# Kernel optimization log

Hardware: AMD Instinct MI355X
Metric: run time of the kernel (lower is better)

## Reference

```python
import jax, jax.numpy as jnp
import numpy as np

E = 8  # num_experts

def setup_inputs() -> dict:
    key = jax.random.key(0)
    ks = jax.random.split(key, 6)
    b, s, d, f = 4, 1024, 1024, 4096
    return {
        "x": jax.random.normal(ks[0], (b, s, d), jnp.float32),
        "Wr": jax.random.normal(ks[1], (d, E), jnp.float32) * 0.02,
        "br": jnp.zeros((E,), jnp.float32),
        "W1": jax.random.normal(ks[2], (E, d, f), jnp.float32) * 0.02,
        "b1": jnp.zeros((E, f), jnp.float32),
        "W2": jax.random.normal(ks[3], (E, f, d), jnp.float32) * 0.02,
        "b2": jnp.zeros((E, d), jnp.float32),
        "k": 2,
    }

def reference(x, Wr, br, W1, b1, W2, b2, k):
    # Router: linear -> softmax -> keep top-k gate probs per token (zero elsewhere).
    # (Gaussian routing noise is a train-time stochastic term; omitted for a
    # deterministic eval-mode reference.)
    logits = jnp.einsum('bsd,de->bse', x, Wr) + br          # [b,s,E]
    probs = jax.nn.softmax(logits, axis=-1)                 # [b,s,E]
    kth = jax.lax.top_k(probs, k)[0][..., -1:]              # [b,s,1]
    gates = jnp.where(probs >= kth, probs, 0.0)             # [b,s,E] sparse gate values
    g = jnp.transpose(gates, (2, 0, 1))[..., None]          # exp_masks [E,b,s,1]

    # Mask-then-dense expert compute, exactly as the torch module:
    # expert_input = x * (mask > 0); out = MLP(expert_input) * gate; sum over experts.
    xm = x[None] * (g > 0).astype(x.dtype)                  # [E,b,s,d]
    h = jax.nn.gelu(jnp.einsum('ebsd,edf->ebsf', xm, W1) + b1[:, None, None, :],
                    approximate=False)                      # [E,b,s,4d]
    out = jnp.einsum('ebsf,efd->ebsd', h, W2) + b2[:, None, None, :]
    out = out * g                                           # gate the expert outputs
    return jnp.sum(out, axis=0)                             # 'sum' aggregation -> [b,s,d]
```

## Files before the change

### kernel.cpp

```cpp
#include <hip/hip_runtime.h>
#include <math.h>

#define T_TOK 4096
#define DDIM  1024
#define FDIM  4096
#define NEXP  8
#define HCAP  8448

typedef __attribute__((ext_vector_type(8))) short bf16x8;
typedef __attribute__((ext_vector_type(4))) float f32x4;

__device__ __forceinline__ unsigned short f2bf(float f) {
  unsigned int u = __float_as_uint(f);
  u += 0x7fffu + ((u >> 16) & 1u);
  return (unsigned short)(u >> 16);
}

__global__ void transpose_cvt_kernel(const float* __restrict__ src,
                                     unsigned short* __restrict__ dst,
                                     int R, int C) {
  __shared__ float tile[32][33];
  int e = blockIdx.z;
  int c0 = blockIdx.x * 32, r0 = blockIdx.y * 32;
  const float* s = src + (size_t)e * R * C;
  unsigned short* d = dst + (size_t)e * R * C;
  int tx = threadIdx.x, ty = threadIdx.y;
#pragma unroll
  for (int i = 0; i < 32; i += 8)
    tile[ty + i][tx] = s[(size_t)(r0 + ty + i) * C + (c0 + tx)];
  __syncthreads();
#pragma unroll
  for (int i = 0; i < 32; i += 8)
    d[(size_t)(c0 + ty + i) * R + (r0 + tx)] = f2bf(tile[tx][ty + i]);
}

__global__ void router_kernel(const float* __restrict__ x, const float* __restrict__ Wr,
                              const float* __restrict__ br, const int* __restrict__ kptr,
                              unsigned short* __restrict__ x_bf,
                              int* __restrict__ counts, int* __restrict__ ids,
                              float* __restrict__ gatev) {
  int t = blockIdx.x * 4 + (threadIdx.x >> 6);
  int lane = threadIdx.x & 63;
  const float* xr = x + (size_t)t * DDIM;
  float acc[NEXP];
#pragma unroll
  for (int e = 0; e < NEXP; ++e) acc[e] = 0.f;
#pragma unroll
  for (int i = 0; i < DDIM / 64; ++i) {
    int idx = lane + 64 * i;
    float xv = xr[idx];
    x_bf[(size_t)t * DDIM + idx] = f2bf(xv);
    const float* wr = Wr + (size_t)idx * NEXP;
#pragma unroll
    for (int e = 0; e < NEXP; ++e) acc[e] += xv * wr[e];
  }
#pragma unroll
  for (int e = 0; e < NEXP; ++e) {
    float v = acc[e];
    for (int off = 32; off > 0; off >>= 1) v += __shfl_xor(v, off);
    acc[e] = v;
  }
  if (lane == 0) {
    float logits[NEXP], probs[NEXP];
    float m = -1e30f;
#pragma unroll
    for (int e = 0; e < NEXP; ++e) { logits[e] = acc[e] + br[e]; m = fmaxf(m, logits[e]); }
    float s = 0.f;
#pragma unroll
    for (int e = 0; e < NEXP; ++e) { probs[e] = expf(logits[e] - m); s += probs[e]; }
    float inv = 1.f / s;
#pragma unroll
    for (int e = 0; e < NEXP; ++e) probs[e] *= inv;
    int kk = *kptr;
    float tmp[NEXP];
#pragma unroll
    for (int e = 0; e < NEXP; ++e) tmp[e] = probs[e];
    float kth = 2.f;
    for (int j = 0; j < kk; ++j) {
      int bi = 0; float bv = -1.f;
#pragma unroll
      for (int e = 0; e < NEXP; ++e)
        if (tmp[e] > bv) { bv = tmp[e]; bi = e; }
      kth = bv; tmp[bi] = -1.f;
    }
#pragma unroll
    for (int e = 0; e < NEXP; ++e) {
      if (probs[e] >= kth) {
        int pos = atomicAdd(&counts[e], 1);
        if (pos < T_TOK) { ids[e * T_TOK + pos] = t; gatev[e * T_TOK + pos] = probs[e]; }
      }
    }
  }
}

__global__ void offsets_kernel(const int* __restrict__ counts, int* __restrict__ hbase) {
  if (threadIdx.x == 0 && blockIdx.x == 0) {
    int s = 0;
    for (int e = 0; e < NEXP; ++e) { hbase[e] = s; s += counts[e]; }
  }
}

__global__ void __launch_bounds__(256) gemm1_kernel(
    const unsigned short* __restrict__ x_bf,
    const unsigned short* __restrict__ W1t,
    const float* __restrict__ b1,
    const int* __restrict__ counts, const int* __restrict__ hbase,
    const int* __restrict__ ids,
    unsigned short* __restrict__ h) {
  int e = blockIdx.z;
  int n_e = counts[e];
  int mt = blockIdx.y;
  if (mt * 128 >= n_e) return;
  int nt = blockIdx.x;
  const unsigned short* Bt = W1t + (size_t)e * FDIM * DDIM;
  __shared__ unsigned short ldsA[128 * 32];
  __shared__ unsigned short ldsB[128 * 32];
  int tid = threadIdx.x;

  const unsigned short* asrc[2];
  const unsigned short* bsrc[2];
  int loff[2];
#pragma unroll
  for (int j = 0; j < 2; ++j) {
    int id = tid + j * 256;
    int row = id >> 2;
    int col = (id & 3) * 8;
    loff[j] = row * 32 + col;
    int gm = mt * 128 + row;
    if (gm > n_e - 1) gm = n_e - 1;
    int tok = ids[e * T_TOK + gm];
    asrc[j] = x_bf + (size_t)tok * DDIM + col;
    bsrc[j] = Bt + (size_t)(nt * 128 + row) * DDIM + col;
  }

  f32x4 acc[4][4];
#pragma unroll
  for (int mi = 0; mi < 4; ++mi)
#pragma unroll
    for (int ni = 0; ni < 4; ++ni) acc[mi][ni] = {0.f, 0.f, 0.f, 0.f};

  int wave = tid >> 6, lane = tid & 63;
  int wm = (wave >> 1) * 64, wn = (wave & 1) * 64;
  int l16 = lane & 15, q = lane >> 4;

  for (int k0 = 0; k0 < DDIM; k0 += 32) {
#pragma unroll
    for (int j = 0; j < 2; ++j) {
      uint4 av = *(const uint4*)(asrc[j] + k0);
      uint4 bv = *(const uint4*)(bsrc[j] + k0);
      *(uint4*)&ldsA[loff[j]] = av;
      *(uint4*)&ldsB[loff[j]] = bv;
    }
    __syncthreads();
    bf16x8 af[4], bfr[4];
#pragma unroll
    for (int mi = 0; mi < 4; ++mi)
      af[mi] = *(const bf16x8*)&ldsA[(wm + mi * 16 + l16) * 32 + q * 8];
#pragma unroll
    for (int ni = 0; ni < 4; ++ni)
      bfr[ni] = *(const bf16x8*)&ldsB[(wn + ni * 16 + l16) * 32 + q * 8];
#pragma unroll
    for (int mi = 0; mi < 4; ++mi)
#pragma unroll
      for (int ni = 0; ni < 4; ++ni)
        acc[mi][ni] = __builtin_amdgcn_mfma_f32_16x16x32_bf16(af[mi], bfr[ni], acc[mi][ni], 0, 0, 0);
    __syncthreads();
  }

  int base = hbase[e];
#pragma unroll
  for (int mi = 0; mi < 4; ++mi) {
#pragma unroll
    for (int r = 0; r < 4; ++r) {
      int rl = wm + mi * 16 + q * 4 + r;
      int gm = mt * 128 + rl;
      if (gm >= n_e) continue;
      int hr = base + gm;
      if (hr >= HCAP) continue;
#pragma unroll
      for (int ni = 0; ni < 4; ++ni) {
        int col = nt * 128 + wn + ni * 16 + l16;
        float v = acc[mi][ni][r] + b1[e * FDIM + col];
        float g = 0.5f * v * (1.0f + erff(v * 0.70710678118654752440f));
        h[(size_t)hr * FDIM + col] = f2bf(g);
      }
    }
  }
}

__global__ void __launch_bounds__(256) gemm2_kernel(
    const unsigned short* __restrict__ h,
    const unsigned short* __restrict__ W2t,
    const float* __restrict__ b2,
    const int* __restrict__ counts, const int* __restrict__ hbase,
    const int* __restrict__ ids, const float* __restrict__ gatev,
    float* __restrict__ out) {
  int e = blockIdx.z;
  int n_e = counts[e];
  int mt = blockIdx.y;
  if (mt * 128 >= n_e) return;
  int nt = blockIdx.x;
  const unsigned short* Bt = W2t + (size_t)e * DDIM * FDIM;
  int base = hbase[e];
  __shared__ unsigned short ldsA[128 * 32];
  __shared__ unsigned short ldsB[128 * 32];
  int tid = threadIdx.x;

  const unsigned short* asrc[2];
  const unsigned short* bsrc[2];
  int loff[2];
#pragma unroll
  for (int j = 0; j < 2; ++j) {
    int id = tid + j * 256;
    int row = id >> 2;
    int col = (id & 3) * 8;
    loff[j] = row * 32 + col;
    int gm = mt * 128 + row;
    if (gm > n_e - 1) gm = n_e - 1;
    int hr = base + gm;
    if (hr > HCAP - 1) hr = HCAP - 1;
    asrc[j] = h + (size_t)hr * FDIM + col;
    bsrc[j] = Bt + (size_t)(nt * 128 + row) * FDIM + col;
  }

  f32x4 acc[4][4];
#pragma unroll
  for (int mi = 0; mi < 4; ++mi)
#pragma unroll
    for (int ni = 0; ni < 4; ++ni) acc[mi][ni] = {0.f, 0.f, 0.f, 0.f};

  int wave = tid >> 6, lane = tid & 63;
  int wm = (wave >> 1) * 64, wn = (wave & 1) * 64;
  int l16 = lane & 15, q = lane >> 4;

  for (int k0 = 0; k0 < FDIM; k0 += 32) {
#pragma unroll
    for (int j = 0; j < 2; ++j) {
      uint4 av = *(const uint4*)(asrc[j] + k0);
      uint4 bv = *(const uint4*)(bsrc[j] + k0);
      *(uint4*)&ldsA[loff[j]] = av;
      *(uint4*)&ldsB[loff[j]] = bv;
    }
    __syncthreads();
    bf16x8 af[4], bfr[4];
#pragma unroll
    for (int mi = 0; mi < 4; ++mi)
      af[mi] = *(const bf16x8*)&ldsA[(wm + mi * 16 + l16) * 32 + q * 8];
#pragma unroll
    for (int ni = 0; ni < 4; ++ni)
      bfr[ni] = *(const bf16x8*)&ldsB[(wn + ni * 16 + l16) * 32 + q * 8];
#pragma unroll
    for (int mi = 0; mi < 4; ++mi)
#pragma unroll
      for (int ni = 0; ni < 4; ++ni)
        acc[mi][ni] = __builtin_amdgcn_mfma_f32_16x16x32_bf16(af[mi], bfr[ni], acc[mi][ni], 0, 0, 0);
    __syncthreads();
  }

#pragma unroll
  for (int mi = 0; mi < 4; ++mi) {
#pragma unroll
    for (int r = 0; r < 4; ++r) {
      int rl = wm + mi * 16 + q * 4 + r;
      int gm = mt * 128 + rl;
      if (gm >= n_e) continue;
      int tok = ids[e * T_TOK + gm];
      float g = gatev[e * T_TOK + gm];
#pragma unroll
      for (int ni = 0; ni < 4; ++ni) {
        int col = nt * 128 + wn + ni * 16 + l16;
        float v = g * (acc[mi][ni][r] + b2[e * DDIM + col]);
        atomicAdd(&out[(size_t)tok * DDIM + col], v);
      }
    }
  }
}

extern "C" void kernel_launch(void* const* d_in, const int* in_sizes, int n_in,
                              void* d_out, int out_size, void* d_ws, size_t ws_size,
                              hipStream_t stream) {
  const float* x  = (const float*)d_in[0];
  const float* Wr = (const float*)d_in[1];
  const float* br = (const float*)d_in[2];
  const float* W1 = (const float*)d_in[3];
  const float* b1 = (const float*)d_in[4];
  const float* W2 = (const float*)d_in[5];
  const float* b2 = (const float*)d_in[6];
  const int* kptr = (const int*)d_in[7];
  float* out = (float*)d_out;

  char* ws = (char*)d_ws;
  size_t o = 0;
  unsigned short* x_bf = (unsigned short*)(ws + o); o += (size_t)T_TOK * DDIM * 2;
  unsigned short* W1t  = (unsigned short*)(ws + o); o += (size_t)NEXP * FDIM * DDIM * 2;
  unsigned short* W2t  = (unsigned short*)(ws + o); o += (size_t)NEXP * DDIM * FDIM * 2;
  unsigned short* hbuf = (unsigned short*)(ws + o); o += (size_t)HCAP * FDIM * 2;
  int*   ids    = (int*)(ws + o);   o += (size_t)NEXP * T_TOK * 4;
  float* gatev  = (float*)(ws + o); o += (size_t)NEXP * T_TOK * 4;
  int*   counts = (int*)(ws + o);   o += 64;
  int*   hbase  = (int*)(ws + o);   o += 64;
  if (o > ws_size) return;

  hipMemsetAsync(d_out, 0, (size_t)out_size * 4, stream);
  hipMemsetAsync(counts, 0, 128, stream);

  transpose_cvt_kernel<<<dim3(FDIM / 32, DDIM / 32, NEXP), dim3(32, 8), 0, stream>>>(W1, W1t, DDIM, FDIM);
  transpose_cvt_kernel<<<dim3(DDIM / 32, FDIM / 32, NEXP), dim3(32, 8), 0, stream>>>(W2, W2t, FDIM, DDIM);

  router_kernel<<<T_TOK / 4, 256, 0, stream>>>(x, Wr, br, kptr, x_bf, counts, ids, gatev);
  offsets_kernel<<<1, 64, 0, stream>>>(counts, hbase);

  gemm1_kernel<<<dim3(FDIM / 128, T_TOK / 128, NEXP), 256, 0, stream>>>(
      x_bf, W1t, b1, counts, hbase, ids, hbuf);
  gemm2_kernel<<<dim3(DDIM / 128, T_TOK / 128, NEXP), 256, 0, stream>>>(
      hbuf, W2t, b2, counts, hbase, ids, gatev, out);
}
```

Before: 752.3 us.

## Use direct global-to-LDS loads and split-K the second expert GEMM

Replaces the register-staged global→LDS tile copies in both expert GEMMs with the global_load_lds builtin, so loads go straight into shared memory without a VGPR round trip. gemm2 is split along the F dimension into two chunks, doubling the grid so more workgroups run at once, with the bias added only by the first chunk and partial results combined through the existing atomicAdd. This adds more atomic traffic to the output and relies on the async LDS load finishing before the existing barrier, with no explicit wait on vmcnt.

```diff
diff --git a/kernel.cpp b/kernel.cpp
--- a/kernel.cpp
+++ b/kernel.cpp
@@ -14,6 +14,13 @@
   unsigned int u = __float_as_uint(f);
   u += 0x7fffu + ((u >> 16) & 1u);
   return (unsigned short)(u >> 16);
+}
+
+__device__ __forceinline__ void async_copy16(const unsigned short* gsrc, unsigned short* ldst) {
+  __builtin_amdgcn_global_load_lds(
+      (const __attribute__((address_space(1))) unsigned int*)gsrc,
+      (__attribute__((address_space(3))) unsigned int*)ldst,
+      16, 0, 0);
 }
 
 __global__ void transpose_cvt_kernel(const float* __restrict__ src,
@@ -146,10 +153,8 @@
   for (int k0 = 0; k0 < DDIM; k0 += 32) {
 #pragma unroll
     for (int j = 0; j < 2; ++j) {
-      uint4 av = *(const uint4*)(asrc[j] + k0);
-      uint4 bv = *(const uint4*)(bsrc[j] + k0);
-      *(uint4*)&ldsA[loff[j]] = av;
-      *(uint4*)&ldsB[loff[j]] = bv;
+      async_copy16(asrc[j] + k0, &ldsA[loff[j]]);
+      async_copy16(bsrc[j] + k0, &ldsB[loff[j]]);
     }
     __syncthreads();
     bf16x8 af[4], bfr[4];
@@ -188,6 +193,8 @@
   }
 }
 
+#define KSPLIT 2
+#define KCHUNK (FDIM / KSPLIT)
 __global__ void __launch_bounds__(256) gemm2_kernel(
     const unsigned short* __restrict__ h,
     const unsigned short* __restrict__ W2t,
@@ -195,12 +202,13 @@
     const int* __restrict__ counts, const int* __restrict__ hbase,
     const int* __restrict__ ids, const float* __restrict__ gatev,
     float* __restrict__ out) {
-  int e = blockIdx.z;
+  int e = blockIdx.z >> 1;
+  int kc = blockIdx.z & 1;
   int n_e = counts[e];
   int mt = blockIdx.y;
   if (mt * 128 >= n_e) return;
   int nt = blockIdx.x;
-  const unsigned short* Bt = W2t + (size_t)e * DDIM * FDIM;
+  const unsigned short* Bt = W2t + (size_t)e * DDIM * FDIM + kc * KCHUNK;
   int base = hbase[e];
   __shared__ unsigned short ldsA[128 * 32];
   __shared__ unsigned short ldsB[128 * 32];
@@ -219,7 +227,7 @@
     if (gm > n_e - 1) gm = n_e - 1;
     int hr = base + gm;
     if (hr > HCAP - 1) hr = HCAP - 1;
-    asrc[j] = h + (size_t)hr * FDIM + col;
+    asrc[j] = h + (size_t)hr * FDIM + kc * KCHUNK + col;
     bsrc[j] = Bt + (size_t)(nt * 128 + row) * FDIM + col;
   }
 
@@ -233,13 +241,11 @@
   int wm = (wave >> 1) * 64, wn = (wave & 1) * 64;
   int l16 = lane & 15, q = lane >> 4;
 
-  for (int k0 = 0; k0 < FDIM; k0 += 32) {
+  for (int k0 = 0; k0 < KCHUNK; k0 += 32) {
 #pragma unroll
     for (int j = 0; j < 2; ++j) {
-      uint4 av = *(const uint4*)(asrc[j] + k0);
-      uint4 bv = *(const uint4*)(bsrc[j] + k0);
-      *(uint4*)&ldsA[loff[j]] = av;
-      *(uint4*)&ldsB[loff[j]] = bv;
+      async_copy16(asrc[j] + k0, &ldsA[loff[j]]);
+      async_copy16(bsrc[j] + k0, &ldsB[loff[j]]);
     }
     __syncthreads();
     bf16x8 af[4], bfr[4];
@@ -269,7 +275,8 @@
 #pragma unroll
       for (int ni = 0; ni < 4; ++ni) {
         int col = nt * 128 + wn + ni * 16 + l16;
-        float v = g * (acc[mi][ni][r] + b2[e * DDIM + col]);
+        float bias = (kc == 0) ? b2[e * DDIM + col] : 0.f;
+        float v = g * (acc[mi][ni][r] + bias);
         atomicAdd(&out[(size_t)tok * DDIM + col], v);
       }
     }
@@ -312,6 +319,6 @@
 
   gemm1_kernel<<<dim3(FDIM / 128, T_TOK / 128, NEXP), 256, 0, stream>>>(
       x_bf, W1t, b1, counts, hbase, ids, hbuf);
-  gemm2_kernel<<<dim3(DDIM / 128, T_TOK / 128, NEXP), 256, 0, stream>>>(
+  gemm2_kernel<<<dim3(DDIM / 128, T_TOK / 128, NEXP * KSPLIT), 256, 0, stream>>>(
       hbuf, W2t, b2, counts, hbase, ids, gatev, out);
 }
```

After: 745.6 us. No clear change (-0.9%).
